# Performance work log

Hardware: AMD Instinct MI355X
Metric: run time of the kernel (lower is better)

The kernel has to match this reference:

```python
import jax, jax.numpy as jnp
import numpy as np

N = 50000   # total nodes across batched graphs
E = 800000  # total edges
F = 30      # input node features
G = 256     # number of graphs in the disjoint batch
CH = [128, 64, 32]
N_LABELS = 2


def setup_inputs() -> dict:
    key = jax.random.key(0)
    ks = jax.random.split(key, 16)
    x = jax.random.normal(ks[0], (N, F), dtype=jnp.float32)
    edge_weight = jax.random.uniform(ks[1], (E,), dtype=jnp.float32)
    edge_row = jax.random.randint(ks[2], (E,), 0, N, dtype=jnp.int32)
    edge_col = jax.random.randint(ks[3], (E,), 0, N, dtype=jnp.int32)
    seg = jnp.sort(jax.random.randint(ks[4], (N,), 0, G, dtype=jnp.int32))
    # GCSConv params: out = A @ (x W1) + x W2 + b, per layer
    dims = [F] + CH
    params = {}
    kk = 5
    for l in range(3):
        fin, fout = dims[l], dims[l + 1]
        s = 1.0 / np.sqrt(fin)
        params[f"w1_{l+1}"] = jax.random.uniform(ks[kk], (fin, fout), minval=-s, maxval=s, dtype=jnp.float32); kk += 1
        params[f"w2_{l+1}"] = jax.random.uniform(ks[kk], (fin, fout), minval=-s, maxval=s, dtype=jnp.float32); kk += 1
        params[f"b_{l+1}"] = jnp.zeros((fout,), dtype=jnp.float32)
    sd = 1.0 / np.sqrt(CH[-1])
    params["wd"] = jax.random.uniform(ks[kk], (CH[-1], N_LABELS), minval=-sd, maxval=sd, dtype=jnp.float32)
    params["bd"] = jnp.zeros((N_LABELS,), dtype=jnp.float32)
    return {"x": x, "edge_weight": edge_weight, "edge_row": edge_row,
            "edge_col": edge_col, "seg": seg, **params}


def _gcs_conv(x, ew, er, ec, w1, w2, b):
    # spektral GCSConv: relu(A @ (x W1) + x W2 + b) with sparse A in COO form
    h = x @ w1                                   # [N, Fout]
    msgs = ew[:, None] * h[ec]                   # gather along edges [E, Fout]
    agg = jax.ops.segment_sum(msgs, er, num_segments=N)  # SpMM scatter [N, Fout]
    return jax.nn.relu(agg + x @ w2 + b)


def reference(x, edge_weight, edge_row, edge_col, seg,
              w1_1, w2_1, b_1, w1_2, w2_2, b_2, w1_3, w2_3, b_3, wd, bd):
    h = _gcs_conv(x, edge_weight, edge_row, edge_col, w1_1, w2_1, b_1)
    h = _gcs_conv(h, edge_weight, edge_row, edge_col, w1_2, w2_2, b_2)
    h = _gcs_conv(h, edge_weight, edge_row, edge_col, w1_3, w2_3, b_3)
    # GlobalAvgPool: segment mean over graph ids
    sums = jax.ops.segment_sum(h, seg, num_segments=G)               # [G, 32]
    cnts = jax.ops.segment_sum(jnp.ones((N,), h.dtype), seg, num_segments=G)
    pooled = sums / jnp.maximum(cnts, 1.0)[:, None]
    return jax.nn.softmax(pooled @ wd + bd, axis=-1)                 # [G, 2]
```

## Files before the change

### kernel.cpp

```cpp
#include <hip/hip_runtime.h>
#include <hip/hip_fp16.h>

#define N_NODES 50000
#define N_EDGES 800000
#define N_GRAPHS 256
#define NCB 196
#define CHUNK 3125
#define MBLK 782

typedef _Float16 f16x8 __attribute__((ext_vector_type(8)));
typedef float    f32x4 __attribute__((ext_vector_type(4)));

__global__ __launch_bounds__(256)
void hist_prep(const int* __restrict__ ER, const float* __restrict__ X,
               const int* __restrict__ SEG,
               const float* __restrict__ W1, const float* __restrict__ W2,
               const float* __restrict__ W12, const float* __restrict__ W22,
               const float* __restrict__ W13, const float* __restrict__ W23,
               int* __restrict__ ghist, __half* __restrict__ XPh,
               int* __restrict__ start,
               __half* __restrict__ W1f, __half* __restrict__ W2f,
               __half* __restrict__ W3f)
{
    int b = blockIdx.x;
    int t = threadIdx.x;
    if (b < 256) {
        __shared__ int h[NCB];
        for (int i = t; i < NCB; i += 256) h[i] = 0;
        __syncthreads();
        int lo = b * CHUNK, hi = lo + CHUNK;
        for (int e = lo + t; e < hi; e += 256) atomicAdd(&h[ER[e] >> 8], 1);
        __syncthreads();
        for (int i = t; i < NCB; i += 256) ghist[i * 256 + b] = h[i];
        return;
    }
    int bid = b - 256;
    if (bid < 782) {
        int idx = bid * 256 + t;
        int n = idx >> 2;
        int c4 = idx & 3;
        if (n >= N_NODES) return;
        __half2 hb[4];
        #pragma unroll
        for (int k = 0; k < 4; ++k) {
            int c0 = c4 * 8 + 2 * k;
            float v0 = (c0 < 30) ? X[n * 30 + c0] : 0.f;
            float v1 = (c0 + 1 < 30) ? X[n * 30 + c0 + 1] : 0.f;
            hb[k] = __float22half2_rn(make_float2(v0, v1));
        }
        *(uint4*)(XPh + (size_t)n * 32 + c4 * 8) = *(uint4*)&hb[0];
    } else if (bid < 978) {
        int n = (bid - 782) * 256 + t;
        if (n >= N_NODES) return;
        int g = SEG[n];
        int gprev = (n == 0) ? -1 : SEG[n - 1];
        for (int gg = gprev + 1; gg <= g; ++gg) start[gg] = n;
        if (n == N_NODES - 1)
            for (int gg = g + 1; gg <= N_GRAPHS; ++gg) start[gg] = N_NODES;
    } else {
        int idx = (bid - 978) * 256 + t;
        if (idx < 8192) {
            int i = idx & 7, c = (idx >> 3) & 15, g = (idx >> 7) & 3;
            int s = (idx >> 9) & 1, n = idx >> 10;
            int k = s * 32 + g * 8 + i, col = n * 16 + c;
            float w = 0.f;
            if (k < 30) w = W1[k * 128 + col];
            else if (k >= 32 && k < 62) w = W2[(k - 32) * 128 + col];
            W1f[idx] = __float2half(w);
        } else if (idx < 24576) {
            int o = idx - 8192;
            int i = o & 7, c = (o >> 3) & 15, g = (o >> 7) & 3;
            int s = (o >> 9) & 3, n = o >> 11;
            int k = s * 32 + g * 8 + i, col = n * 16 + c;
            float w = (col < 64) ? W12[k * 64 + col] : W22[k * 64 + col - 64];
            W2f[o] = __float2half(w);
        } else {
            int o = idx - 24576;
            int i = o & 7, c = (o >> 3) & 15, g = (o >> 7) & 3;
            int s = (o >> 9) & 1, n = o >> 10;
            int k = s * 32 + g * 8 + i, col = n * 16 + c;
            float w = (col < 32) ? W13[k * 32 + col] : W23[k * 32 + col - 32];
            W3f[o] = __float2half(w);
        }
    }
}

__global__ __launch_bounds__(256)
void scan1(int* __restrict__ ghist, int* __restrict__ bsum)
{
    __shared__ int s[256];
    int t = threadIdx.x, b = blockIdx.x;
    int i = b * 256 + t;
    int v = ghist[i];
    s[t] = v;
    __syncthreads();
    for (int off = 1; off < 256; off <<= 1) {
        int u = (t >= off) ? s[t - off] : 0;
        __syncthreads();
        s[t] += u;
        __syncthreads();
    }
    ghist[i] = s[t] - v;
    if (t == 255) bsum[b] = s[255];
}

__global__ __launch_bounds__(256)
void c_scatter(const int* __restrict__ ER, const int* __restrict__ EC,
               const float* __restrict__ EW, const int* __restrict__ ghist,
               const int* __restrict__ bsum, uint2* __restrict__ tmp)
{
    __shared__ int s[256];
    __shared__ int cur[NCB];
    int t = threadIdx.x, blk = blockIdx.x;
    int v = (t < NCB) ? bsum[t] : 0;
    s[t] = v;
    __syncthreads();
    for (int off = 1; off < 256; off <<= 1) {
        int u = (t >= off) ? s[t - off] : 0;
        __syncthreads();
        s[t] += u;
        __syncthreads();
    }
    if (t < NCB) cur[t] = (s[t] - v) + ghist[t * 256 + blk];
    __syncthreads();
    int lo = blk * CHUNK, hi = lo + CHUNK;
    for (int e = lo + t; e < hi; e += 256) {
        int d = ER[e];
        int pos = atomicAdd(&cur[d >> 8], 1);
        tmp[pos] = make_uint2((unsigned int)EC[e] | ((unsigned int)(d & 255) << 16),
                              (unsigned int)__half_as_ushort(__float2half(EW[e])));
    }
}

__device__ __forceinline__ void fma8h(float4& a0, float4& a1, float w,
                                      const uint4& raw)
{
    const __half2* hp = (const __half2*)&raw;
    float2 f0 = __half22float2(hp[0]);
    float2 f1 = __half22float2(hp[1]);
    float2 f2 = __half22float2(hp[2]);
    float2 f3 = __half22float2(hp[3]);
    a0.x = fmaf(w, f0.x, a0.x); a0.y = fmaf(w, f0.y, a0.y);
    a0.z = fmaf(w, f1.x, a0.z); a0.w = fmaf(w, f1.y, a0.w);
    a1.x = fmaf(w, f2.x, a1.x); a1.y = fmaf(w, f2.y, a1.y);
    a1.z = fmaf(w, f3.x, a1.z); a1.w = fmaf(w, f3.y, a1.w);
}

__global__ __launch_bounds__(1024)
void bsort(const uint2* __restrict__ tmp, const int* __restrict__ bsum,
           unsigned int* __restrict__ packed, int* __restrict__ rowptr)
{
    __shared__ int s[256];
    __shared__ int hist[256];
    __shared__ int cur[256];
    int t = threadIdx.x, b = blockIdx.x;

    if (t < 256) s[t] = (t < NCB) ? bsum[t] : 0;
    __syncthreads();
    for (int off = 1; off < 256; off <<= 1) {
        int u = 0;
        if (t < 256 && t >= off) u = s[t - off];
        __syncthreads();
        if (t < 256) s[t] += u;
        __syncthreads();
    }
    int cntb = bsum[b];
    int base = s[b] - cntb;
    int end  = base + cntb;
    __syncthreads();

    if (t < 256) hist[t] = 0;
    __syncthreads();
    for (int j = base + t; j < end; j += 1024)
        atomicAdd(&hist[(tmp[j].x >> 16) & 255], 1);
    __syncthreads();
    int hv = 0;
    if (t < 256) { hv = hist[t]; s[t] = hv; }
    __syncthreads();
    for (int off = 1; off < 256; off <<= 1) {
        int u = 0;
        if (t < 256 && t >= off) u = s[t - off];
        __syncthreads();
        if (t < 256) s[t] += u;
        __syncthreads();
    }
    if (t < 256) {
        int excl = s[t] - hv;
        int n = b * 256 + t;
        if (n < N_NODES) rowptr[n] = base + excl;
        if (b == NCB - 1 && t == 0) rowptr[N_NODES] = N_EDGES;
        cur[t] = base + excl;
    }
    __syncthreads();
    for (int j = base + t; j < end; j += 1024) {
        uint2 v = tmp[j];
        int pos = atomicAdd(&cur[(v.x >> 16) & 255], 1);
        packed[pos] = (v.x & 0xFFFF) | (v.y << 16);
    }
}

__global__ __launch_bounds__(512)
void dense12_mfma(const __half* __restrict__ XPh, const int* __restrict__ rowptr,
                  const unsigned int* __restrict__ packed,
                  const __half* __restrict__ W1f, const float* __restrict__ B1,
                  const __half* __restrict__ W2f, const float* __restrict__ B2,
                  __half* __restrict__ H2h, __half* __restrict__ A2h)
{
    __shared__ __align__(16) __half As[64 * 72];
    __shared__ __align__(16) __half Hs[64 * 136];
    const int tid = threadIdx.x;
    const int m0 = blockIdx.x * 64;

    if (tid < 256) {
        int row = tid >> 2, c4 = tid & 3;
        int gm = m0 + row;
        uint4 v = make_uint4(0, 0, 0, 0);
        if (gm < N_NODES) v = *(const uint4*)(XPh + (size_t)gm * 32 + c4 * 8);
        *(uint4*)(As + row * 72 + (4 + c4) * 8) = v;
    }
    {
        int local = tid >> 3;
        int es = (tid >> 2) & 1;
        int q = tid & 3;
        int n = m0 + local;
        float4 acc0 = make_float4(0.f, 0.f, 0.f, 0.f);
        float4 acc1 = make_float4(0.f, 0.f, 0.f, 0.f);
        if (n < N_NODES) {
            int r0 = rowptr[n], r1 = rowptr[n + 1];
            int mid = (r0 + r1) >> 1;
            int lo = es ? mid : r0;
            int hi = es ? r1 : mid;
            int j = lo;
            for (; j + 3 < hi; j += 4) {
                unsigned int ra = packed[j],     rb = packed[j + 1];
                unsigned int rc = packed[j + 2], rd = packed[j + 3];
                uint4 rawa = *(const uint4*)(XPh + (size_t)(ra & 0xFFFF) * 32 + q * 8);
                uint4 rawb = *(const uint4*)(XPh + (size_t)(rb & 0xFFFF) * 32 + q * 8);
                uint4 rawc = *(const uint4*)(XPh + (size_t)(rc & 0xFFFF) * 32 + q * 8);
                uint4 rawd = *(const uint4*)(XPh + (size_t)(rd & 0xFFFF) * 32 + q * 8);
                float wa = __half2float(__ushort_as_half((unsigned short)(ra >> 16)));
                float wb = __half2float(__ushort_as_half((unsigned short)(rb >> 16)));
                float wc = __half2float(__ushort_as_half((unsigned short)(rc >> 16)));
                float wd = __half2float(__ushort_as_half((unsigned short)(rd >> 16)));
                fma8h(acc0, acc1, wa, rawa);
                fma8h(acc0, acc1, wb, rawb);
                fma8h(acc0, acc1, wc, rawc);
                fma8h(acc0, acc1, wd, rawd);
            }
            for (; j < hi; ++j) {
                unsigned int r = packed[j];
                uint4 raw = *(const uint4*)(XPh + (size_t)(r & 0xFFFF) * 32 + q * 8);
                float wv = __half2float(__ushort_as_half((unsigned short)(r >> 16)));
                fma8h(acc0, acc1, wv, raw);
            }
        }
        float* part = (float*)Hs;
        if (es == 1) {
            *(float4*)&part[local * 36 + q * 8 + 0] = acc0;
            *(float4*)&part[local * 36 + q * 8 + 4] = acc1;
        }
        __syncthreads();
        if (es == 0) {
            float4 p0 = *(float4*)&part[local * 36 + q * 8 + 0];
            float4 p1 = *(float4*)&part[local * 36 + q * 8 + 4];
            acc0.x += p0.x; acc0.y += p0.y; acc0.z += p0.z; acc0.w += p0.w;
            acc1.x += p1.x; acc1.y += p1.y; acc1.z += p1.z; acc1.w += p1.w;
            __half2 hb2[4];
            hb2[0] = __float22half2_rn(make_float2(acc0.x, acc0.y));
            hb2[1] = __float22half2_rn(make_float2(acc0.z, acc0.w));
            hb2[2] = __float22half2_rn(make_float2(acc1.x, acc1.y));
            hb2[3] = __float22half2_rn(make_float2(acc1.z, acc1.w));
            *(uint4*)(As + local * 72 + q * 8) = *(uint4*)&hb2[0];
        }
    }
    __syncthreads();

    const int lane = tid & 63;
    const int w  = tid >> 6;
    const int lr = lane & 15;
    const int lg = lane >> 4;

    f32x4 acc[4];
    #pragma unroll
    for (int m = 0; m < 4; ++m) acc[m] = (f32x4){0.f, 0.f, 0.f, 0.f};

    #pragma unroll
    for (int s = 0; s < 2; ++s) {
        f16x8 b = *(const f16x8*)(W1f + (((w * 2 + s) * 4 + lg) * 16 + lr) * 8);
        #pragma unroll
        for (int m = 0; m < 4; ++m) {
            f16x8 a = *(const f16x8*)(As + (m * 16 + lr) * 72 + s * 32 + lg * 8);
            acc[m] = __builtin_amdgcn_mfma_f32_16x16x32_f16(a, b, acc[m], 0, 0, 0);
        }
    }

    {
        const float bias = B1[w * 16 + lr];
        #pragma unroll
        for (int m = 0; m < 4; ++m)
            #pragma unroll
            for (int r = 0; r < 4; ++r) {
                float v = fmaxf(acc[m][r] + bias, 0.f);
                Hs[(m * 16 + lg * 4 + r) * 136 + w * 16 + lr] = __float2half(v);
            }
    }
    __syncthreads();

    f32x4 acc2[4];
    #pragma unroll
    for (int m = 0; m < 4; ++m) acc2[m] = (f32x4){0.f, 0.f, 0.f, 0.f};

    #pragma unroll
    for (int s = 0; s < 4; ++s) {
        f16x8 b = *(const f16x8*)(W2f + (((w * 4 + s) * 4 + lg) * 16 + lr) * 8);
        #pragma unroll
        for (int m = 0; m < 4; ++m) {
            f16x8 a = *(const f16x8*)(Hs + (m * 16 + lr) * 136 + s * 32 + lg * 8);
            acc2[m] = __builtin_amdgcn_mfma_f32_16x16x32_f16(a, b, acc2[m], 0, 0, 0);
        }
    }
    __syncthreads();

    {
        const float bias = (w >= 4) ? B2[(w - 4) * 16 + lr] : 0.f;
        #pragma unroll
        for (int m = 0; m < 4; ++m)
            #pragma unroll
            for (int r = 0; r < 4; ++r)
                Hs[(m * 16 + lg * 4 + r) * 136 + w * 16 + lr] =
                    __float2half(acc2[m][r] + bias);
    }
    __syncthreads();

    for (int idx = tid; idx < 1024; idx += 512) {
        int row = idx >> 4, c8 = idx & 15;
        int gm = m0 + row;
        if (gm < N_NODES) {
            uint4 v = *(const uint4*)(Hs + row * 136 + c8 * 8);
            if (c8 < 8) *(uint4*)(H2h + (size_t)gm * 64 + c8 * 8) = v;
            else        *(uint4*)(A2h + (size_t)gm * 64 + (c8 - 8) * 8) = v;
        }
    }
}

__global__ __launch_bounds__(1024)
void spmm_dense3(const __half* __restrict__ H2h, const int* __restrict__ rowptr,
                 const unsigned int* __restrict__ packed,
                 const __half* __restrict__ A2h, const __half* __restrict__ W3f,
                 const float* __restrict__ B3, __half* __restrict__ H3h,
                 __half* __restrict__ B2h)
{
    __shared__ __align__(16) __half As[64 * 72];
    __shared__ __align__(16) __half Os[64 * 72];
    __shared__ float part[64][68];
    const int tid = threadIdx.x;
    const int m0 = blockIdx.x * 64;

    {
        int local = tid >> 4;
        int es = (tid >> 3) & 1;
        int q = tid & 7;
        int n = m0 + local;
        float4 acc0 = make_float4(0.f, 0.f, 0.f, 0.f);
        float4 acc1 = make_float4(0.f, 0.f, 0.f, 0.f);
        if (n < N_NODES) {
            int r0 = rowptr[n], r1 = rowptr[n + 1];
            int mid = (r0 + r1) >> 1;
            int lo = es ? mid : r0;
            int hi = es ? r1 : mid;
            if (es == 0) {
                uint4 raw = *(const uint4*)(A2h + (size_t)n * 64 + q * 8);
                const __half2* hp = (const __half2*)&raw;
                float2 f0 = __half22float2(hp[0]);
                float2 f1 = __half22float2(hp[1]);
                float2 f2 = __half22float2(hp[2]);
                float2 f3 = __half22float2(hp[3]);
                acc0 = make_float4(f0.x, f0.y, f1.x, f1.y);
                acc1 = make_float4(f2.x, f2.y, f3.x, f3.y);
            }
            int j = lo;
            for (; j + 3 < hi; j += 4) {
                unsigned int ra = packed[j],     rb = packed[j + 1];
                unsigned int rc = packed[j + 2], rd = packed[j + 3];
                uint4 rawa = *(const uint4*)(H2h + (size_t)(ra & 0xFFFF) * 64 + q * 8);
                uint4 rawb = *(const uint4*)(H2h + (size_t)(rb & 0xFFFF) * 64 + q * 8);
                uint4 rawc = *(const uint4*)(H2h + (size_t)(rc & 0xFFFF) * 64 + q * 8);
                uint4 rawd = *(const uint4*)(H2h + (size_t)(rd & 0xFFFF) * 64 + q * 8);
                float wa = __half2float(__ushort_as_half((unsigned short)(ra >> 16)));
                float wb = __half2float(__ushort_as_half((unsigned short)(rb >> 16)));
                float wc = __half2float(__ushort_as_half((unsigned short)(rc >> 16)));
                float wd = __half2float(__ushort_as_half((unsigned short)(rd >> 16)));
                fma8h(acc0, acc1, wa, rawa);
                fma8h(acc0, acc1, wb, rawb);
                fma8h(acc0, acc1, wc, rawc);
                fma8h(acc0, acc1, wd, rawd);
            }
            for (; j < hi; ++j) {
                unsigned int r = packed[j];
                uint4 raw = *(const uint4*)(H2h + (size_t)(r & 0xFFFF) * 64 + q * 8);
                float w = __half2float(__ushort_as_half((unsigned short)(r >> 16)));
                fma8h(acc0, acc1, w, raw);
            }
        }
        if (es == 1) {
            *(float4*)&part[local][q * 8 + 0] = acc0;
            *(float4*)&part[local][q * 8 + 4] = acc1;
        }
        __syncthreads();
        if (es == 0) {
            float4 p0 = *(float4*)&part[local][q * 8 + 0];
            float4 p1 = *(float4*)&part[local][q * 8 + 4];
            acc0.x += p0.x; acc0.y += p0.y; acc0.z += p0.z; acc0.w += p0.w;
            acc1.x += p1.x; acc1.y += p1.y; acc1.z += p1.z; acc1.w += p1.w;
            __half2 hb[4];
            hb[0] = __float22half2_rn(make_float2(fmaxf(acc0.x, 0.f), fmaxf(acc0.y, 0.f)));
            hb[1] = __float22half2_rn(make_float2(fmaxf(acc0.z, 0.f), fmaxf(acc0.w, 0.f)));
            hb[2] = __float22half2_rn(make_float2(fmaxf(acc1.x, 0.f), fmaxf(acc1.y, 0.f)));
            hb[3] = __float22half2_rn(make_float2(fmaxf(acc1.z, 0.f), fmaxf(acc1.w, 0.f)));
            *(uint4*)(As + local * 72 + q * 8) = *(uint4*)&hb[0];
        }
    }
    __syncthreads();

    const int lane = tid & 63;
    const int w  = tid >> 6;
    const int wm = w >> 2;
    const int wn = w & 3;
    const int lr = lane & 15;
    const int lg = lane >> 4;

    f32x4 acc = (f32x4){0.f, 0.f, 0.f, 0.f};
    #pragma unroll
    for (int s = 0; s < 2; ++s) {
        f16x8 b = *(const f16x8*)(W3f + (((wn * 2 + s) * 4 + lg) * 16 + lr) * 8);
        f16x8 a = *(const f16x8*)(As + (wm * 16 + lr) * 72 + s * 32 + lg * 8);
        acc = __builtin_amdgcn_mfma_f32_16x16x32_f16(a, b, acc, 0, 0, 0);
    }

    const float bias = (wn >= 2) ? B3[(wn - 2) * 16 + lr] : 0.f;
    #pragma unroll
    for (int r = 0; r < 4; ++r)
        Os[(wm * 16 + lg * 4 + r) * 72 + wn * 16 + lr] = __float2half(acc[r] + bias);
    __syncthreads();

    if (tid < 512) {
        int row = tid >> 3, c8 = tid & 7;
        int gm = m0 + row;
        if (gm < N_NODES) {
            uint4 v = *(const uint4*)(Os + row * 72 + c8 * 8);
            if (c8 < 4) *(uint4*)(H3h + (size_t)gm * 32 + c8 * 8) = v;
            else        *(uint4*)(B2h + (size_t)gm * 32 + (c8 - 4) * 8) = v;
        }
    }
}

template<int FOUT, int S>
__global__ __launch_bounds__(512)
void spmm_split(const __half* __restrict__ H, const int* __restrict__ rowptr,
                const unsigned int* __restrict__ packed, __half* __restrict__ AGGh)
{
    constexpr int T = FOUT / 8;
    constexpr int NPB = 512 / (S * T);
    __shared__ float part[NPB][S - 1][FOUT + 4];
    int tid = threadIdx.x;
    int local = tid / (S * T);
    int rem = tid % (S * T);
    int s = rem / T;
    int q = rem % T;
    int n = blockIdx.x * NPB + local;
    bool valid = (n < N_NODES);
    float4 acc0 = make_float4(0.f, 0.f, 0.f, 0.f);
    float4 acc1 = make_float4(0.f, 0.f, 0.f, 0.f);
    __half* ap = AGGh + (size_t)n * FOUT + q * 8;
    if (valid) {
        int r0 = rowptr[n], r1 = rowptr[n + 1];
        int deg = r1 - r0;
        int lo = r0 + (deg * s) / S;
        int hi = r0 + (deg * (s + 1)) / S;
        if (s == 0) {
            uint4 raw = *(const uint4*)ap;
            const __half2* hp = (const __half2*)&raw;
            float2 f0 = __half22float2(hp[0]);
            float2 f1 = __half22float2(hp[1]);
            float2 f2 = __half22float2(hp[2]);
            float2 f3 = __half22float2(hp[3]);
            acc0 = make_float4(f0.x, f0.y, f1.x, f1.y);
            acc1 = make_float4(f2.x, f2.y, f3.x, f3.y);
        }
        int j = lo;
        for (; j + 3 < hi; j += 4) {
            unsigned int ra = packed[j],     rb = packed[j + 1];
            unsigned int rc = packed[j + 2], rd = packed[j + 3];
            uint4 rawa = *(const uint4*)(H + (size_t)(ra & 0xFFFF) * FOUT + q * 8);
            uint4 rawb = *(const uint4*)(H + (size_t)(rb & 0xFFFF) * FOUT + q * 8);
            uint4 rawc = *(const uint4*)(H + (size_t)(rc & 0xFFFF) * FOUT + q * 8);
            uint4 rawd = *(const uint4*)(H + (size_t)(rd & 0xFFFF) * FOUT + q * 8);
            float wa = __half2float(__ushort_as_half((unsigned short)(ra >> 16)));
            float wb = __half2float(__ushort_as_half((unsigned short)(rb >> 16)));
            float wc = __half2float(__ushort_as_half((unsigned short)(rc >> 16)));
            float wd = __half2float(__ushort_as_half((unsigned short)(rd >> 16)));
            fma8h(acc0, acc1, wa, rawa);
            fma8h(acc0, acc1, wb, rawb);
            fma8h(acc0, acc1, wc, rawc);
            fma8h(acc0, acc1, wd, rawd);
        }
        for (; j < hi; ++j) {
            unsigned int r = packed[j];
            uint4 raw = *(const uint4*)(H + (size_t)(r & 0xFFFF) * FOUT + q * 8);
            float w = __half2float(__ushort_as_half((unsigned short)(r >> 16)));
            fma8h(acc0, acc1, w, raw);
        }
    }
    if (s > 0) {
        *(float4*)&part[local][s - 1][q * 8 + 0] = acc0;
        *(float4*)&part[local][s - 1][q * 8 + 4] = acc1;
    }
    __syncthreads();
    if (s == 0 && valid) {
        #pragma unroll
        for (int ss = 0; ss < S - 1; ++ss) {
            float4 p0 = *(float4*)&part[local][ss][q * 8 + 0];
            float4 p1 = *(float4*)&part[local][ss][q * 8 + 4];
            acc0.x += p0.x; acc0.y += p0.y; acc0.z += p0.z; acc0.w += p0.w;
            acc1.x += p1.x; acc1.y += p1.y; acc1.z += p1.z; acc1.w += p1.w;
        }
        __half2 hb[4];
        hb[0] = __float22half2_rn(make_float2(acc0.x, acc0.y));
        hb[1] = __float22half2_rn(make_float2(acc0.z, acc0.w));
        hb[2] = __float22half2_rn(make_float2(acc1.x, acc1.y));
        hb[3] = __float22half2_rn(make_float2(acc1.z, acc1.w));
        *(uint4*)ap = *(uint4*)&hb[0];
    }
}

__global__ __launch_bounds__(1024)
void pool_kernel(const __half* __restrict__ H, const int* __restrict__ start,
                 const float* __restrict__ WD, const float* __restrict__ BD,
                 float* __restrict__ OUT)
{
    __shared__ float red[32][33];
    int g = blockIdx.x;
    int s = start[g], e = start[g + 1];
    int q = threadIdx.x & 31;
    int grp = threadIdx.x >> 5;
    float acc = 0.f;
    for (int n = s + grp; n < e; n += 32)
        acc += fmaxf(__half2float(H[(size_t)n * 32 + q]), 0.f);
    red[grp][q] = acc;
    __syncthreads();
    if (threadIdx.x < 32) {
        float v = 0.f;
        #pragma unroll
        for (int i = 0; i < 32; ++i) v += red[i][q];
        float inv = (e > s) ? 1.0f / (float)(e - s) : 1.0f;
        float p = v * inv;
        float p0 = p * WD[q * 2 + 0];
        float p1 = p * WD[q * 2 + 1];
        #pragma unroll
        for (int off = 16; off; off >>= 1) {
            p0 += __shfl_down(p0, off, 32);
            p1 += __shfl_down(p1, off, 32);
        }
        if (q == 0) {
            float l0 = p0 + BD[0], l1 = p1 + BD[1];
            float m = fmaxf(l0, l1);
            float e0 = expf(l0 - m), e1 = expf(l1 - m);
            float si = 1.0f / (e0 + e1);
            OUT[g * 2 + 0] = e0 * si;
            OUT[g * 2 + 1] = e1 * si;
        }
    }
}

extern "C" void kernel_launch(void* const* d_in, const int* in_sizes, int n_in,
                              void* d_out, int out_size, void* d_ws, size_t ws_size,
                              hipStream_t stream)
{
    const float* x    = (const float*)d_in[0];
    const float* ew   = (const float*)d_in[1];
    const int*   er   = (const int*)d_in[2];
    const int*   ec   = (const int*)d_in[3];
    const int*   seg  = (const int*)d_in[4];
    const float* w1_1 = (const float*)d_in[5];
    const float* w2_1 = (const float*)d_in[6];
    const float* b_1  = (const float*)d_in[7];
    const float* w1_2 = (const float*)d_in[8];
    const float* w2_2 = (const float*)d_in[9];
    const float* b_2  = (const float*)d_in[10];
    const float* w1_3 = (const float*)d_in[11];
    const float* w2_3 = (const float*)d_in[12];
    const float* b_3  = (const float*)d_in[13];
    const float* wd   = (const float*)d_in[14];
    const float* bd   = (const float*)d_in[15];

    float* ws = (float*)d_ws;
    int*   IW = (int*)d_ws;
    __half* XPh    = (__half*)ws;
    uint2*  tmp    = (uint2*)(ws + 1600000);
    __half* H2h    = (__half*)(ws + 3200000);
    __half* A2h    = (__half*)(ws + 4800000);
    __half* H3h    = (__half*)(ws + 6400000);
    __half* B2h    = (__half*)(ws + 7200000);
    unsigned int* packed = (unsigned int*)(IW + 8000000);
    int*    rowptr = IW + 9000000;
    int*    ghist  = IW + 9060000;
    int*    bsum   = IW + 9115000;
    int*    start  = IW + 9120000;
    __half* W1f    = (__half*)(ws + 9125000);
    __half* W2f    = (__half*)(ws + 9130000);
    __half* W3f    = (__half*)(ws + 9139000);

    dim3 blk(256);

    hist_prep<<<dim3(256 + 782 + 196 + 112), blk, 0, stream>>>(
        er, x, seg, w1_1, w2_1, w1_2, w2_2, w1_3, w2_3,
        ghist, XPh, start, W1f, W2f, W3f);
    scan1<<<dim3(NCB), blk, 0, stream>>>(ghist, bsum);
    c_scatter<<<dim3(256), blk, 0, stream>>>(er, ec, ew, ghist, bsum, tmp);
    bsort<<<dim3(NCB), dim3(1024), 0, stream>>>(tmp, bsum, packed, rowptr);

    dense12_mfma<<<dim3(MBLK), dim3(512), 0, stream>>>(XPh, rowptr, packed,
                                                       W1f, b_1, W2f, b_2,
                                                       H2h, A2h);
    spmm_dense3<<<dim3(MBLK), dim3(1024), 0, stream>>>(H2h, rowptr, packed, A2h,
                                                       W3f, b_3, H3h, B2h);
    spmm_split<32, 4><<<dim3((N_NODES + 31) / 32), dim3(512), 0, stream>>>(H3h, rowptr,
                                                                           packed, B2h);

    pool_kernel<<<dim3(N_GRAPHS), dim3(1024), 0, stream>>>(B2h, start, wd, bd,
                                                           (float*)d_out);
}
```

Before: 166.6 us.

## Fuse final SpMM layer with graph pooling via shared and global atomics

Merges the last-layer sparse aggregation and the global average pool into one kernel. Each block reduces its ReLU'd node rows into per-graph partial sums in shared memory, then atomically adds those into a global per-graph buffer that is zeroed in the prep kernel. A small single-block head kernel applies the mean, dense layer and softmax. This drops the fp16 write and re-read of the final activations and one launch, at the cost of float atomics and non-deterministic summation order.

```diff
diff --git a/kernel.cpp b/kernel.cpp
--- a/kernel.cpp
+++ b/kernel.cpp
@@ -20,7 +20,7 @@
                int* __restrict__ ghist, __half* __restrict__ XPh,
                int* __restrict__ start,
                __half* __restrict__ W1f, __half* __restrict__ W2f,
-               __half* __restrict__ W3f)
+               __half* __restrict__ W3f, float* __restrict__ PS)
 {
     int b = blockIdx.x;
     int t = threadIdx.x;
@@ -57,7 +57,7 @@
         for (int gg = gprev + 1; gg <= g; ++gg) start[gg] = n;
         if (n == N_NODES - 1)
             for (int gg = g + 1; gg <= N_GRAPHS; ++gg) start[gg] = N_NODES;
-    } else {
+    } else if (bid < 1090) {
         int idx = (bid - 978) * 256 + t;
         if (idx < 8192) {
             int i = idx & 7, c = (idx >> 3) & 15, g = (idx >> 7) & 3;
@@ -82,6 +82,9 @@
             float w = (col < 32) ? W13[k * 32 + col] : W23[k * 32 + col - 32];
             W3f[o] = __float2half(w);
         }
+    } else {
+        int idx = (bid - 1090) * 256 + t;
+        PS[idx] = 0.f;
     }
 }
 
@@ -454,31 +457,33 @@
     }
 }
 
-template<int FOUT, int S>
-__global__ __launch_bounds__(512)
-void spmm_split(const __half* __restrict__ H, const int* __restrict__ rowptr,
-                const unsigned int* __restrict__ packed, __half* __restrict__ AGGh)
-{
-    constexpr int T = FOUT / 8;
-    constexpr int NPB = 512 / (S * T);
-    __shared__ float part[NPB][S - 1][FOUT + 4];
-    int tid = threadIdx.x;
-    int local = tid / (S * T);
-    int rem = tid % (S * T);
-    int s = rem / T;
-    int q = rem % T;
-    int n = blockIdx.x * NPB + local;
+__global__ __launch_bounds__(1024)
+void spmm_pool(const __half* __restrict__ H, const int* __restrict__ rowptr,
+               const unsigned int* __restrict__ packed,
+               const __half* __restrict__ Bse, const int* __restrict__ SEG,
+               float* __restrict__ PS)
+{
+    __shared__ float part[64][3][36];
+    __shared__ float ps[65][32];
+    const int tid = threadIdx.x;
+    const int n0 = blockIdx.x * 64;
+
+    for (int i = tid; i < 65 * 32; i += 1024) ((float*)ps)[i] = 0.f;
+
+    int local = tid >> 4;
+    int s = (tid >> 2) & 3;
+    int q = tid & 3;
+    int n = n0 + local;
     bool valid = (n < N_NODES);
     float4 acc0 = make_float4(0.f, 0.f, 0.f, 0.f);
     float4 acc1 = make_float4(0.f, 0.f, 0.f, 0.f);
-    __half* ap = AGGh + (size_t)n * FOUT + q * 8;
     if (valid) {
         int r0 = rowptr[n], r1 = rowptr[n + 1];
         int deg = r1 - r0;
-        int lo = r0 + (deg * s) / S;
-        int hi = r0 + (deg * (s + 1)) / S;
+        int lo = r0 + (deg * s) / 4;
+        int hi = r0 + (deg * (s + 1)) / 4;
         if (s == 0) {
-            uint4 raw = *(const uint4*)ap;
+            uint4 raw = *(const uint4*)(Bse + (size_t)n * 32 + q * 8);
             const __half2* hp = (const __half2*)&raw;
             float2 f0 = __half22float2(hp[0]);
             float2 f1 = __half22float2(hp[1]);
@@ -491,10 +496,10 @@
         for (; j + 3 < hi; j += 4) {
             unsigned int ra = packed[j],     rb = packed[j + 1];
             unsigned int rc = packed[j + 2], rd = packed[j + 3];
-            uint4 rawa = *(const uint4*)(H + (size_t)(ra & 0xFFFF) * FOUT + q * 8);
-            uint4 rawb = *(const uint4*)(H + (size_t)(rb & 0xFFFF) * FOUT + q * 8);
-            uint4 rawc = *(const uint4*)(H + (size_t)(rc & 0xFFFF) * FOUT + q * 8);
-            uint4 rawd = *(const uint4*)(H + (size_t)(rd & 0xFFFF) * FOUT + q * 8);
+            uint4 rawa = *(const uint4*)(H + (size_t)(ra & 0xFFFF) * 32 + q * 8);
+            uint4 rawb = *(const uint4*)(H + (size_t)(rb & 0xFFFF) * 32 + q * 8);
+            uint4 rawc = *(const uint4*)(H + (size_t)(rc & 0xFFFF) * 32 + q * 8);
+            uint4 rawd = *(const uint4*)(H + (size_t)(rd & 0xFFFF) * 32 + q * 8);
             float wa = __half2float(__ushort_as_half((unsigned short)(ra >> 16)));
             float wb = __half2float(__ushort_as_half((unsigned short)(rb >> 16)));
             float wc = __half2float(__ushort_as_half((unsigned short)(rc >> 16)));
@@ -506,7 +511,7 @@
         }
         for (; j < hi; ++j) {
             unsigned int r = packed[j];
-            uint4 raw = *(const uint4*)(H + (size_t)(r & 0xFFFF) * FOUT + q * 8);
+            uint4 raw = *(const uint4*)(H + (size_t)(r & 0xFFFF) * 32 + q * 8);
             float w = __half2float(__ushort_as_half((unsigned short)(r >> 16)));
             fma8h(acc0, acc1, w, raw);
         }
@@ -516,60 +521,57 @@
         *(float4*)&part[local][s - 1][q * 8 + 4] = acc1;
     }
     __syncthreads();
+    int g0 = SEG[n0];
     if (s == 0 && valid) {
         #pragma unroll
-        for (int ss = 0; ss < S - 1; ++ss) {
+        for (int ss = 0; ss < 3; ++ss) {
             float4 p0 = *(float4*)&part[local][ss][q * 8 + 0];
             float4 p1 = *(float4*)&part[local][ss][q * 8 + 4];
             acc0.x += p0.x; acc0.y += p0.y; acc0.z += p0.z; acc0.w += p0.w;
             acc1.x += p1.x; acc1.y += p1.y; acc1.z += p1.z; acc1.w += p1.w;
         }
-        __half2 hb[4];
-        hb[0] = __float22half2_rn(make_float2(acc0.x, acc0.y));
-        hb[1] = __float22half2_rn(make_float2(acc0.z, acc0.w));
-        hb[2] = __float22half2_rn(make_float2(acc1.x, acc1.y));
-        hb[3] = __float22half2_rn(make_float2(acc1.z, acc1.w));
-        *(uint4*)ap = *(uint4*)&hb[0];
-    }
-}
-
-__global__ __launch_bounds__(1024)
-void pool_kernel(const __half* __restrict__ H, const int* __restrict__ start,
+        float* dst = &ps[SEG[n] - g0][q * 8];
+        atomicAdd(&dst[0], fmaxf(acc0.x, 0.f));
+        atomicAdd(&dst[1], fmaxf(acc0.y, 0.f));
+        atomicAdd(&dst[2], fmaxf(acc0.z, 0.f));
+        atomicAdd(&dst[3], fmaxf(acc0.w, 0.f));
+        atomicAdd(&dst[4], fmaxf(acc1.x, 0.f));
+        atomicAdd(&dst[5], fmaxf(acc1.y, 0.f));
+        atomicAdd(&dst[6], fmaxf(acc1.z, 0.f));
+        atomicAdd(&dst[7], fmaxf(acc1.w, 0.f));
+    }
+    __syncthreads();
+    int nlast = n0 + 63;
+    if (nlast >= N_NODES) nlast = N_NODES - 1;
+    int span = SEG[nlast] - g0 + 1;
+    for (int i = tid; i < span * 32; i += 1024) {
+        float v = ps[i >> 5][i & 31];
+        if (v != 0.f)
+            atomicAdd(&PS[(size_t)(g0 + (i >> 5)) * 32 + (i & 31)], v);
+    }
+}
+
+__global__ __launch_bounds__(256)
+void head_kernel(const float* __restrict__ PS, const int* __restrict__ start,
                  const float* __restrict__ WD, const float* __restrict__ BD,
                  float* __restrict__ OUT)
 {
-    __shared__ float red[32][33];
-    int g = blockIdx.x;
+    int g = threadIdx.x;
     int s = start[g], e = start[g + 1];
-    int q = threadIdx.x & 31;
-    int grp = threadIdx.x >> 5;
-    float acc = 0.f;
-    for (int n = s + grp; n < e; n += 32)
-        acc += fmaxf(__half2float(H[(size_t)n * 32 + q]), 0.f);
-    red[grp][q] = acc;
-    __syncthreads();
-    if (threadIdx.x < 32) {
-        float v = 0.f;
-        #pragma unroll
-        for (int i = 0; i < 32; ++i) v += red[i][q];
-        float inv = (e > s) ? 1.0f / (float)(e - s) : 1.0f;
-        float p = v * inv;
-        float p0 = p * WD[q * 2 + 0];
-        float p1 = p * WD[q * 2 + 1];
-        #pragma unroll
-        for (int off = 16; off; off >>= 1) {
-            p0 += __shfl_down(p0, off, 32);
-            p1 += __shfl_down(p1, off, 32);
-        }
-        if (q == 0) {
-            float l0 = p0 + BD[0], l1 = p1 + BD[1];
-            float m = fmaxf(l0, l1);
-            float e0 = expf(l0 - m), e1 = expf(l1 - m);
-            float si = 1.0f / (e0 + e1);
-            OUT[g * 2 + 0] = e0 * si;
-            OUT[g * 2 + 1] = e1 * si;
-        }
-    }
+    float inv = (e > s) ? 1.0f / (float)(e - s) : 1.0f;
+    float l0 = 0.f, l1 = 0.f;
+    #pragma unroll
+    for (int j = 0; j < 32; ++j) {
+        float p = PS[g * 32 + j] * inv;
+        l0 = fmaf(p, WD[j * 2 + 0], l0);
+        l1 = fmaf(p, WD[j * 2 + 1], l1);
+    }
+    l0 += BD[0]; l1 += BD[1];
+    float m = fmaxf(l0, l1);
+    float e0 = expf(l0 - m), e1 = expf(l1 - m);
+    float si = 1.0f / (e0 + e1);
+    OUT[g * 2 + 0] = e0 * si;
+    OUT[g * 2 + 1] = e1 * si;
 }
 
 extern "C" void kernel_launch(void* const* d_in, const int* in_sizes, int n_in,
@@ -609,12 +611,13 @@
     __half* W1f    = (__half*)(ws + 9125000);
     __half* W2f    = (__half*)(ws + 9130000);
     __half* W3f    = (__half*)(ws + 9139000);
+    float*  PS     = ws + 9145000;
 
     dim3 blk(256);
 
-    hist_prep<<<dim3(256 + 782 + 196 + 112), blk, 0, stream>>>(
+    hist_prep<<<dim3(256 + 782 + 196 + 112 + 32), blk, 0, stream>>>(
         er, x, seg, w1_1, w2_1, w1_2, w2_2, w1_3, w2_3,
-        ghist, XPh, start, W1f, W2f, W3f);
+        ghist, XPh, start, W1f, W2f, W3f, PS);
     scan1<<<dim3(NCB), blk, 0, stream>>>(ghist, bsum);
     c_scatter<<<dim3(256), blk, 0, stream>>>(er, ec, ew, ghist, bsum, tmp);
     bsort<<<dim3(NCB), dim3(1024), 0, stream>>>(tmp, bsum, packed, rowptr);
@@ -624,9 +627,7 @@
                                                        H2h, A2h);
     spmm_dense3<<<dim3(MBLK), dim3(1024), 0, stream>>>(H2h, rowptr, packed, A2h,
                                                        W3f, b_3, H3h, B2h);
-    spmm_split<32, 4><<<dim3((N_NODES + 31) / 32), dim3(512), 0, stream>>>(H3h, rowptr,
-                                                                           packed, B2h);
-
-    pool_kernel<<<dim3(N_GRAPHS), dim3(1024), 0, stream>>>(B2h, start, wd, bd,
-                                                           (float*)d_out);
-}
+    spmm_pool<<<dim3(MBLK), dim3(1024), 0, stream>>>(H3h, rowptr, packed, B2h,
+                                                     seg, PS);
+    head_kernel<<<dim3(1), blk, 0, stream>>>(PS, start, wd, bd, (float*)d_out);
+}
```

Result: slower. 177.0 us (+6.3%).
